# Kernel optimization log

Hardware: AMD Instinct MI355X
Metric: run time of the kernel (lower is better)

The kernel has to match this reference:

```python
import jax, jax.numpy as jnp
import numpy as np

B, L, NV = 16, 512, 321
D, PL, ST = 128, 16, 8
P = (L - PL) // ST + 2  # 64 patches (replication pad of `stride` on the right)
E, K, H = 8, 2, 512     # experts, top-n gates, expert hidden (4*d_model)
PRED = 96
BAL_COEF, Z_COEF = 0.01, 0.001


def sinusoidal_pe(n, d):
    pos = np.arange(n)[:, None].astype(np.float32)
    div = np.exp(np.arange(0, d, 2).astype(np.float32) * -(np.log(10000.0) / d))
    pe = np.zeros((n, d), dtype=np.float32)
    pe[:, 0::2] = np.sin(pos * div)
    pe[:, 1::2] = np.cos(pos * div)
    return jnp.asarray(pe)


def setup_inputs() -> dict:
    key = jax.random.key(0)
    ks = jax.random.split(key, 12)
    s = lambda i, shape, sc: jax.random.normal(ks[i], shape, jnp.float32) * sc
    return {
        "x_enc": jax.random.normal(ks[0], (B, L, NV), jnp.float32),
        "x_mark_enc": jax.random.normal(ks[1], (B, L, 4), jnp.float32),
        "x_dec": jax.random.normal(ks[2], (B, PRED, NV), jnp.float32),
        "x_mark_dec": jax.random.normal(ks[3], (B, PRED, 4), jnp.float32),
        "W_val": s(4, (PL, D), PL ** -0.5),
        "W_g": s(5, (D, E), D ** -0.5),
        "W1": s(6, (E, D, H), D ** -0.5),
        "b1": jnp.zeros((E, H), jnp.float32),
        "W2": s(7, (E, H, D), H ** -0.5),
        "b2": jnp.zeros((E, D), jnp.float32),
        "W_head": s(8, (D * P, PRED), (D * P) ** -0.5),
        "b_head": jnp.zeros((PRED,), jnp.float32),
    }


def _forward(x_enc, W_val, W_g, W1, b1, W2, b2, W_head, b_head):
    # RevIN-style instance norm (means detached as in torch .detach())
    means = jax.lax.stop_gradient(jnp.mean(x_enc, axis=1, keepdims=True))
    xc = x_enc - means
    stdev = jnp.sqrt(jnp.var(xc, axis=1, keepdims=True) + 1e-5)
    xn = xc / stdev

    # Patch embedding: [B, NV, L] -> replicate-pad -> unfold -> linear + sinusoidal PE
    x = jnp.transpose(xn, (0, 2, 1))                        # [B, NV, L]
    x = jnp.pad(x, ((0, 0), (0, 0), (0, ST)), mode="edge")  # ReplicationPad1d((0, stride))
    idx = np.arange(P)[:, None] * ST + np.arange(PL)        # [P, PL]
    patches = x[:, :, idx]                                  # [B, NV, P, PL]
    tok = patches.reshape(B * NV, P, PL)
    emb = tok @ W_val + sinusoidal_pe(P, D)[None]           # [N, P, D]

    # MoE: top-n softmax gating (gates not renormalized), balance + router-z aux losses
    t = emb.reshape(-1, D)                                  # [T, D], T = B*NV*P
    logits = t @ W_g                                        # [T, E]
    probs = jax.nn.softmax(logits, axis=-1)
    topv, topi = jax.lax.top_k(probs, K)                    # [T, K]

    out = jnp.zeros_like(t)
    for e in range(E):  # fixed small expert count; each expert is a GELU MLP
        h = jax.nn.gelu(t @ W1[e] + b1[e], approximate=False) @ W2[e] + b2[e]
        g = jnp.sum(jnp.where(topi == e, topv, 0.0), axis=-1)  # gate for expert e (0 if unrouted)
        out = out + g[:, None] * h

    me = jnp.mean(probs, axis=0)                                            # mean router prob per expert
    ce = jnp.mean(jax.nn.one_hot(topi, E, dtype=probs.dtype).sum(1), 0) / K  # dispatch fraction per expert
    balance_loss = E * jnp.sum(me * ce)
    z_loss = jnp.mean(jax.nn.logsumexp(logits, axis=-1) ** 2)
    aux = BAL_COEF * balance_loss + Z_COEF * z_loss

    # FlattenHead: [B, NV, P, D] -> [B, NV, D, P] -> flatten(-2) -> Linear(nf, pred_len)
    enc = out.reshape(B, NV, P, D).transpose(0, 1, 3, 2)    # [B, NV, D, P]
    dec = enc.reshape(B, NV, D * P) @ W_head + b_head        # [B, NV, PRED]
    dec = jnp.transpose(dec, (0, 2, 1))                      # [B, PRED, NV]

    # de-normalize
    dec = dec * stdev[:, 0][:, None, :] + means[:, 0][:, None, :]
    return dec, aux


def reference(x_enc, x_mark_enc, x_dec, x_mark_dec, W_val, W_g, W1, b1, W2, b2, W_head, b_head):
    return _forward(x_enc, W_val, W_g, W1, b1, W2, b2, W_head, b_head)
```

## Files before the change

kernel.cpp:

```cpp
#include <hip/hip_runtime.h>
#include <hip/hip_bf16.h>

typedef unsigned short u16;
typedef unsigned int   u32;
typedef unsigned long long u64;
typedef __attribute__((ext_vector_type(8))) short bf16x8;
typedef __attribute__((ext_vector_type(4))) float f32x4;
typedef __attribute__((ext_vector_type(16))) float f32x16;
typedef __attribute__((ext_vector_type(2))) unsigned int u32x2;

#define MFMA16(a,b,c) __builtin_amdgcn_mfma_f32_16x16x32_bf16(a,b,c,0,0,0)
#define MFMA32(a,b,c) __builtin_amdgcn_mfma_f32_32x32x16_bf16(a,b,c,0,0,0)

#define NV_   321
#define B_    16
#define L_    512
#define D_    128
#define P_    64
#define E_    8
#define H_    512
#define NRW   5136
#define NTOK  328704
#define DP_   8192
#define NBUCK 329728

static __device__ __forceinline__ u16 f2bf(float f){
  __hip_bfloat16 h = __float2bfloat16(f);
  return *reinterpret_cast<u16*>(&h);
}

static __device__ __forceinline__ float gelu_f(float x){
  float x2 = x*x;
  float p  = __builtin_fmaf(-0.1029433f, x2, -2.3022083f);
  float a  = x*p;
  float en = exp2f(a);
  float r  = __builtin_amdgcn_rcpf(1.0f + en);
  return x*r;
}

static constexpr size_t alup(size_t x){ return (x + 255) & ~(size_t)255; }
static constexpr size_t OFF_MEAN = 0;
static constexpr size_t OFF_RSTD = OFF_MEAN + alup((size_t)NRW*4);
static constexpr size_t OFF_STD  = OFF_RSTD + alup((size_t)NRW*4);
static constexpr size_t OFF_XT   = OFF_STD  + alup((size_t)NRW*4);
static constexpr size_t OFF_PE   = OFF_XT   + alup((size_t)NRW*L_*4);
static constexpr size_t OFF_W1T  = OFF_PE   + alup((size_t)P_*D_*4);
static constexpr size_t OFF_W2T  = OFF_W1T  + alup((size_t)E_*H_*D_*2);
static constexpr size_t OFF_WHT  = OFF_W2T  + alup((size_t)E_*D_*H_*2);
static constexpr size_t OFF_T    = OFF_WHT  + alup((size_t)96*DP_*2);
static constexpr size_t OFF_TOPI = OFF_T    + alup((size_t)NTOK*D_*2);
static constexpr size_t OFF_GATE = OFF_TOPI + alup((size_t)NTOK*4);
static constexpr size_t OFF_CNTR = OFF_GATE + alup((size_t)NTOK*8);
static constexpr size_t OFF_BTOK = OFF_CNTR + alup((size_t)1024);
static constexpr size_t OFF_BGT  = OFF_BTOK + alup((size_t)2*NBUCK*4);
static constexpr size_t OFF_OUT  = OFF_BGT  + alup((size_t)2*NBUCK*4);
static constexpr size_t OFF_MEAND= OFF_OUT  + alup((size_t)NTOK*D_*2);
static constexpr size_t OFF_RSTDD= OFF_MEAND+ alup((size_t)NRW*8);
static constexpr size_t OFF_WVG  = OFF_RSTDD+ alup((size_t)NRW*8);
static constexpr size_t OFF_PEG  = OFF_WVG  + alup((size_t)16*8*8);
static constexpr size_t OFF_PG   = OFF_PEG  + alup((size_t)P_*E_*8);
static constexpr size_t OFF_PI   = OFF_PG   + alup((size_t)NRW*12*4);



__global__ void k_xt(const float* __restrict__ x, float* __restrict__ xT){
  __shared__ float tile[32][33];
  int b = blockIdx.z;
  int v0 = blockIdx.x*32, l0 = blockIdx.y*32;
  int tx = threadIdx.x, ty = threadIdx.y;
  for(int i=ty;i<32;i+=8){
    int l = l0+i, v = v0+tx;
    tile[i][tx] = (v<NV_) ? x[((size_t)b*L_ + l)*NV_ + v] : 0.f;
  }
  __syncthreads();
  for(int i=ty;i<32;i+=8){
    int v = v0+i, l = l0+tx;
    if(v<NV_) xT[((size_t)(b*NV_+v))*L_ + l] = tile[tx][i];
  }
}

__global__ void k_stats(const float* __restrict__ xT, float* meanp, float* rstdp, float* stdp,
                        double* meand, double* rstdd){
  __shared__ double s1[256], s2[256];
  int r = blockIdx.x, t = threadIdx.x;
  double a = (double)xT[(size_t)r*L_ + t], b = (double)xT[(size_t)r*L_ + 256 + t];
  s1[t]=a+b; s2[t]=a*a+b*b;
  __syncthreads();
  for(int o=128;o>0;o>>=1){ if(t<o){ s1[t]+=s1[t+o]; s2[t]+=s2[t+o]; } __syncthreads(); }
  if(t==0){
    double m = s1[0]*(1.0/512.0);
    double var = s2[0]*(1.0/512.0) - m*m;
    double sd = sqrt(var + 1e-5);
    meanp[r]=(float)m; stdp[r]=(float)sd; rstdp[r]=(float)(1.0/sd);
    meand[r]=m; rstdd[r]=1.0/sd;
  }
}

__global__ void k_wprep(const float* __restrict__ Wval, const float* __restrict__ Wg,
                        const float* __restrict__ W1, const float* __restrict__ W2,
                        const float* __restrict__ Wh,
                        float* __restrict__ pef, double* __restrict__ Wvg,
                        double* __restrict__ peg,
                        u16* __restrict__ W1T, u16* __restrict__ W2T,
                        u16* __restrict__ WhT2){
  __shared__ float tile[32][33];
  int b = blockIdx.x;
  int tx = threadIdx.x, ty = threadIdx.y;
  int t = ty*32 + tx;
  if(b == 0){
    for(int i=t;i<8192;i+=256){
      int p = i>>7, d = i&127, k = d>>1;
      double div = exp(-(double)(2*k) * (9.210340371976184 /128.0));
      double ang = (double)p * div;
      double v = (d&1) ? cos(ang) : sin(ang);
      pef[i] = (float)v;
    }
    __syncthreads();
    if(t<128){
      int j = t>>3, e = t&7;
      double acc = 0.0;
      for(int d=0;d<128;d++) acc += (double)Wval[j*128+d] * (double)Wg[d*8+e];
      Wvg[t] = acc;
    }
    for(int q=t;q<512;q+=256){
      int p = q>>3, e = q&7;
      double acc = 0.0;
      for(int d=0;d<128;d++) acc += (double)pef[p*128+d] * (double)Wg[d*8+e];
      peg[q] = acc;
    }
    return;
  }
  if(b < 1025){
    bool isW1 = (b < 513);
    int rem = isW1 ? (b-1) : (b-513);
    int e = rem >> 6, r6 = rem & 63;
    int R = isW1 ? 128 : 512, C = isW1 ? 512 : 128;
    int c0 = (isW1 ? (r6 & 15) : (r6 & 3))*32;
    int r0 = (isW1 ? (r6 >> 4) : (r6 >> 2))*32;
    const float* src = (isW1 ? W1 : W2) + (size_t)e*R*C;
    u16* dst = (isW1 ? W1T : W2T) + (size_t)e*R*C;
    for(int i=ty;i<32;i+=8){
      int r=r0+i, c=c0+tx;
      tile[i][tx] = (r<R && c<C) ? src[(size_t)r*C+c] : 0.f;
    }
    __syncthreads();
    for(int i=ty;i<32;i+=8){
      int c=c0+i, r=r0+tx;
      if(c<C && r<R) dst[(size_t)c*R + r] = f2bf(tile[tx][i]);
    }
    return;
  }
  {
    int rem = b - 1025;
    int p = rem / 12, rr = rem - p*12;
    int d0 = (rr & 3)*32, o0 = (rr >> 2)*32;
    for(int i=ty;i<32;i+=8){
      int r = (d0+i)*64 + p;
      tile[i][tx] = Wh[(size_t)r*96 + o0 + tx];
    }
    __syncthreads();
    for(int i=ty;i<32;i+=8){
      int o = o0+i;
      WhT2[(size_t)o*DP_ + p*128 + d0 + tx] = f2bf(tile[tx][i]);
    }
  }
}

__global__ __launch_bounds__(256) void k_embed(
    const float* __restrict__ xT, const float* __restrict__ meanp, const float* __restrict__ rstdp,
    const float* __restrict__ Wval, const float* __restrict__ pe,
    u16* __restrict__ tglob)
{
  __shared__ __align__(16) float xn[520];
  int r = blockIdx.x, t = threadIdx.x;
  float mean = meanp[r], rstd = rstdp[r];
  float v0 = (xT[(size_t)r*L_ + t]       - mean)*rstd;
  float v1 = (xT[(size_t)r*L_ + 256 + t] - mean)*rstd;
  xn[t] = v0; xn[t+256] = v1;
  if(t==255){
    #pragma unroll
    for(int i=512;i<520;i++) xn[i]=v1;
  }
  int d0 = (t & 63)*2;
  int p0 = t >> 6;
  float2 w[16];
  #pragma unroll
  for(int j=0;j<16;j++) w[j] = *(const float2*)(Wval + j*128 + d0);
  __syncthreads();

  for(int p=p0;p<64;p+=4){
    const float4* xp = (const float4*)(xn + p*8);
    float4 x0=xp[0], x1=xp[1], x2=xp[2], x3=xp[3];
    float xv[16];
    *(float4*)(xv+0)=x0; *(float4*)(xv+4)=x1; *(float4*)(xv+8)=x2; *(float4*)(xv+12)=x3;
    float2 pw = *(const float2*)(pe + p*128 + d0);
    float a0 = pw.x, a1 = pw.y;
    #pragma unroll
    for(int j=0;j<16;j++){ a0 += xv[j]*w[j].x; a1 += xv[j]*w[j].y; }
    u32 packed = (u32)f2bf(a0) | ((u32)f2bf(a1)<<16);
    *(u32*)(tglob + ((size_t)(r*64+p)*128 + d0)) = packed;
  }
}

__global__ __launch_bounds__(256) void k_gate(
    const float* __restrict__ xT, const double* __restrict__ meand, const double* __restrict__ rstdd,
    const double* __restrict__ Wvg, const double* __restrict__ peg,
    int* __restrict__ topip, float2* __restrict__ gatep,
    float* __restrict__ pg, int* __restrict__ pib)
{
  __shared__ double xn[520];
  __shared__ double lgt[64][9];
  int r = blockIdx.x, t = threadIdx.x;
  double m = meand[r], rs = rstdd[r];
  double v0 = ((double)xT[(size_t)r*L_ + t]       - m)*rs;
  double v1 = ((double)xT[(size_t)r*L_ + 256 + t] - m)*rs;
  xn[t]=v0; xn[t+256]=v1;
  if(t==255){
    #pragma unroll
    for(int i=512;i<520;i++) xn[i]=v1;
  }
  __syncthreads();
  for(int q=t;q<512;q+=256){
    int p = q>>3, e = q&7;
    double acc = peg[q];
    #pragma unroll
    for(int j=0;j<16;j++) acc += xn[p*8+j]*Wvg[j*8+e];
    lgt[p][e] = acc;
  }
  __syncthreads();
  if(t<64){
    int token = r*64 + t;
    double l0[8];
    #pragma unroll
    for(int e=0;e<8;e++) l0[e]=lgt[t][e];
    double mx=l0[0];
    #pragma unroll
    for(int e=1;e<8;e++) mx = fmax(mx,l0[e]);
    int i1=0; double b1v=l0[0];
    #pragma unroll
    for(int e=1;e<8;e++) if(l0[e]>b1v){b1v=l0[e]; i1=e;}
    int i2=-1; double b2v=-1e300;
    #pragma unroll
    for(int e=0;e<8;e++) if(e!=i1 && l0[e]>b2v){b2v=l0[e]; i2=e;}
    float pr[8]; float sum=0.f;
    #pragma unroll
    for(int e=0;e<8;e++){ pr[e]=__expf((float)(l0[e]-mx)); sum+=pr[e]; }
    float inv = 1.f/sum;
    #pragma unroll
    for(int e=0;e<8;e++) pr[e]*=inv;
    topip[token] = i1 | (i2<<8);
    gatep[token] = make_float2(pr[i1], pr[i2]);
    float lse = (float)mx + __logf(sum);
    #pragma unroll
    for(int e=0;e<8;e++){
      float v = pr[e];
      for(int o=32;o>0;o>>=1) v += __shfl_down(v,o);
      if(t==0) pg[r*12+e] = v;
    }
    {
      float z = lse*lse;
      for(int o=32;o>0;o>>=1) z += __shfl_down(z,o);
      if(t==0) pg[r*12+8] = z;
    }
    #pragma unroll
    for(int e=0;e<8;e++){
      u64 m1 = __ballot(i1==e);
      u64 m2 = __ballot(i2==e);
      if(t==0){
        pib[r*16+e]   = (int)__popcll(m1);
        pib[r*16+8+e] = (int)__popcll(m2);
      }
    }
  }
}

__global__ __launch_bounds__(256) void k_aux(const float* __restrict__ pg, const int* __restrict__ pib,
                                             int* __restrict__ ci, float* __restrict__ dout){
  __shared__ double sd[256];
  __shared__ int si[256];
  __shared__ double totd[9];
  __shared__ int toti[16];
  int t = threadIdx.x;
  double accd[9]; int acci[16];
  #pragma unroll
  for(int c=0;c<9;c++) accd[c]=0.0;
  #pragma unroll
  for(int c=0;c<16;c++) acci[c]=0;
  for(int r=t;r<NRW;r+=256){
    #pragma unroll
    for(int c=0;c<9;c++) accd[c] += (double)pg[r*12+c];
    #pragma unroll
    for(int c=0;c<16;c++) acci[c] += pib[r*16+c];
  }
  for(int c=0;c<9;c++){
    sd[t]=accd[c]; __syncthreads();
    for(int o=128;o>0;o>>=1){ if(t<o) sd[t]+=sd[t+o]; __syncthreads(); }
    if(t==0) totd[c]=sd[0];
    __syncthreads();
  }
  for(int c=0;c<16;c++){
    si[t]=acci[c]; __syncthreads();
    for(int o=128;o>0;o>>=1){ if(t<o) si[t]+=si[t+o]; __syncthreads(); }
    if(t==0) toti[c]=si[0];
    __syncthreads();
  }
  if(t==0){
    const double invN = 1.0/(double)NTOK;
    double bal = 0.0;
    int es1=0, bs1=0, es2=0, bs2=0;
    for(int e=0;e<8;e++){
      int c1 = toti[e], c2 = toti[8+e];
      bal += (totd[e]*invN) * ((double)(c1+c2) * invN * 0.5);
      ci[32+e]=es1; ci[16+e]=es1; ci[50+e]=bs1;
      ci[41+e]=es2; ci[24+e]=es2; ci[59+e]=bs2;
      es1 += c1; bs1 += (c1+127)>>7;
      es2 += c2; bs2 += (c2+127)>>7;
    }
    ci[40]=es1; ci[58]=bs1;
    ci[49]=es2; ci[67]=bs2;
    dout[493056] = (float)(0.01*8.0*bal + 0.001*(totd[8]*invN));
  }
}

__global__ __launch_bounds__(256) void k_scatter(const int* __restrict__ topip,
    const float2* __restrict__ gatep, int* __restrict__ ci,
    int* __restrict__ btok, float* __restrict__ bgt){
  __shared__ int lc[16]; __shared__ int lb[16];
  int t = threadIdx.x;
  int token = blockIdx.x*256 + t;
  if(t<16) lc[t]=0;
  __syncthreads();
  int ti = topip[token];
  float2 g = gatep[token];
  int e1 = ti & 255, e2 = (ti>>8)&255;
  int r1 = atomicAdd(&lc[e1],1);
  int r2 = atomicAdd(&lc[8+e2],1);
  __syncthreads();
  if(t<8)            lb[t] = atomicAdd(&ci[16+t],   lc[t]);
  else if(t<16)      lb[t] = atomicAdd(&ci[24+t-8], lc[t]);
  __syncthreads();
  int p1 = lb[e1]+r1, p2 = lb[8+e2]+r2;
  btok[p1] = token;         bgt[p1] = g.x;
  btok[NBUCK+p2] = token;   bgt[NBUCK+p2] = g.y;
}

static __device__ __forceinline__ f32x16 acc1_init(const float* b1l, int hc, int hi){
  f32x16 a;
  const float* bp = b1l + hc*32 + 4*hi;
  #pragma unroll
  for(int qq=0;qq<4;qq++){
    f32x4 b4 = *(const f32x4*)(bp + 8*qq);
    a[4*qq+0]=b4.x; a[4*qq+1]=b4.y; a[4*qq+2]=b4.z; a[4*qq+3]=b4.w;
  }
  return a;
}

static __device__ __forceinline__ void gelu_pack(const f32x16& acc1, bf16x8& fA, bf16x8& fB){
  u32 pk[8];
  #pragma unroll
  for(int i=0;i<8;i++){
    float g0 = gelu_f(acc1[2*i]);
    float g1 = gelu_f(acc1[2*i+1]);
    asm("v_cvt_pk_bf16_f32 %0, %1, %2" : "=v"(pk[i]) : "v"(g0), "v"(g1));
  }
  union { bf16x8 v; u32 w[4]; } uA, uB;
  u32x2 s02 = __builtin_amdgcn_permlane32_swap(pk[0], pk[2], false, false);
  u32x2 s13 = __builtin_amdgcn_permlane32_swap(pk[1], pk[3], false, false);
  u32x2 s46 = __builtin_amdgcn_permlane32_swap(pk[4], pk[6], false, false);
  u32x2 s57 = __builtin_amdgcn_permlane32_swap(pk[5], pk[7], false, false);
  uA.w[0]=s02.x; uA.w[1]=s13.x; uA.w[2]=s02.y; uA.w[3]=s13.y;
  uB.w[0]=s46.x; uB.w[1]=s57.x; uB.w[2]=s46.y; uB.w[3]=s57.y;
  fA = uA.v; fB = uB.v;
}

__global__ __launch_bounds__(256,3) void k_expert(
    const u16* __restrict__ tglob,
    const u16* __restrict__ W1T, const u16* __restrict__ W2T,
    const float* __restrict__ b1g, const float* __restrict__ b2g,
    const int* __restrict__ ci,
    const int* __restrict__ btok, const float* __restrict__ bgt,
    u16* __restrict__ outg, int slot)
{
  __shared__ __align__(16) u16 W1b[2][4352];
  __shared__ __align__(16) u16 W2b[2][5120];
  __shared__ __align__(16) float b1l[512];

  int bid = blockIdx.x, t = threadIdx.x;
  int stB = 32 + slot*9, bsB = 50 + slot*9;
  int boff = slot*NBUCK;
  if(bid >= ci[bsB+8]) return;
  int e = 0;
  #pragma unroll
  for(int k2=1;k2<8;k2++) if(bid >= ci[bsB+k2]) e = k2;
  int row0 = ci[stB+e] + (bid - ci[bsB+e])*128;
  int rend = ci[stB+e+1];

  int wid = t>>6, lane = t&63;
  int m = lane&31, hi = lane>>5;
  int rb = wid*32;

  int hr = t>>3, q = t&7;
  int dr = t>>1, q2 = t&1;

  {
    const u16* s1 = W1T + ((size_t)e*H_ + hr)*128 + q*16;
    uint4 p0 = *(const uint4*)(s1);
    uint4 p1 = *(const uint4*)(s1+8);
    u16* d1 = &W1b[0][hr*136 + q*16];
    *(uint4*)(d1)   = p0;
    *(uint4*)(d1+8) = p1;
    if(t<128){
      float4 bv = *(const float4*)(b1g + e*H_ + t*4);
      *(float4*)(b1l + t*4) = bv;
    }
  }

  int posA = row0 + rb + m;
  bool valA = posA < rend;
  int tokA  = valA ? btok[boff+posA] : 0;
  float gt  = valA ? bgt[boff+posA]  : 0.f;
  const u16* arow = tglob + (size_t)tokA*128 + hi*8;
  bf16x8 areg[8];
  #pragma unroll
  for(int ks=0;ks<8;ks++) areg[ks] = *(const bf16x8*)(arow + ks*16);

  f32x16 accO[4];
  #pragma unroll
  for(int nt=0;nt<4;nt++){
    const float* bp2 = b2g + e*D_ + nt*32 + 4*hi;
    #pragma unroll
    for(int qq=0;qq<4;qq++){
      float4 b4 = *(const float4*)(bp2 + 8*qq);
      accO[nt][4*qq+0]=b4.x; accO[nt][4*qq+1]=b4.y;
      accO[nt][4*qq+2]=b4.z; accO[nt][4*qq+3]=b4.w;
    }
  }
  __syncthreads();

  bf16x8 fA, fB;
  {
    const u16* s1 = W1T + ((size_t)e*H_ + 32 + hr)*128 + q*16;
    uint4 l0 = *(const uint4*)(s1), l1 = *(const uint4*)(s1+8);
    const u16* s2 = W2T + ((size_t)e*D_ + dr)*H_ + q2*16;
    uint4 l2 = *(const uint4*)(s2), l3 = *(const uint4*)(s2+8);
    f32x16 acc1 = acc1_init(b1l, 0, hi);
    __builtin_amdgcn_s_setprio(1);
    #pragma unroll
    for(int ks=0;ks<8;ks++){
      bf16x8 wa = *(const bf16x8*)(&W1b[0][0] + m*136 + ks*16 + hi*8);
      acc1 = MFMA32(wa, areg[ks], acc1);
    }
    __builtin_amdgcn_s_setprio(0);
    u16* d1 = &W1b[1][hr*136 + q*16];
    *(uint4*)(d1)   = l0; *(uint4*)(d1+8) = l1;
    u16* d2 = &W2b[0][dr*40 + q2*16];
    *(uint4*)(d2)   = l2; *(uint4*)(d2+8) = l3;
    gelu_pack(acc1, fA, fB);
    __syncthreads();
  }
  for(int hc=1; hc<16; hc++){
    uint4 l0, l1;
    if(hc<15){
      const u16* s1 = W1T + ((size_t)e*H_ + (hc+1)*32 + hr)*128 + q*16;
      l0 = *(const uint4*)(s1); l1 = *(const uint4*)(s1+8);
    }
    const u16* s2 = W2T + ((size_t)e*D_ + dr)*H_ + hc*32 + q2*16;
    uint4 l2 = *(const uint4*)(s2), l3 = *(const uint4*)(s2+8);
    f32x16 acc1 = acc1_init(b1l, hc, hi);
    const u16* W1c = &W1b[hc&1][0];
    const u16* W2p = &W2b[(hc-1)&1][0];
    __builtin_amdgcn_s_setprio(1);
    #pragma unroll
    for(int ks=0;ks<8;ks++){
      bf16x8 wa = *(const bf16x8*)(W1c + m*136 + ks*16 + hi*8);
      acc1 = MFMA32(wa, areg[ks], acc1);
      bf16x8 a2 = *(const bf16x8*)(W2p + ((ks&3)*32+m)*40 + (ks>>2)*16 + hi*8);
      accO[ks&3] = MFMA32(a2, (ks>>2)?fB:fA, accO[ks&3]);
    }
    __builtin_amdgcn_s_setprio(0);
    if(hc<15){
      u16* d1 = &W1b[(hc+1)&1][hr*136 + q*16];
      *(uint4*)(d1)   = l0; *(uint4*)(d1+8) = l1;
    }
    u16* d2 = &W2b[hc&1][dr*40 + q2*16];
    *(uint4*)(d2)   = l2; *(uint4*)(d2+8) = l3;
    gelu_pack(acc1, fA, fB);
    __syncthreads();
  }
  {
    const u16* W2p = &W2b[1][0];
    __builtin_amdgcn_s_setprio(1);
    #pragma unroll
    for(int ks=0;ks<8;ks++){
      bf16x8 a2 = *(const bf16x8*)(W2p + ((ks&3)*32+m)*40 + (ks>>2)*16 + hi*8);
      accO[ks&3] = MFMA32(a2, (ks>>2)?fB:fA, accO[ks&3]);
    }
    __builtin_amdgcn_s_setprio(0);
  }

  if(valA){
    u16* obase = outg + (size_t)tokA*128 + 4*hi;
    #pragma unroll
    for(int nt=0;nt<4;nt++){
      #pragma unroll
      for(int qq=0;qq<4;qq++){
        float v0 = accO[nt][4*qq+0]*gt;
        float v1 = accO[nt][4*qq+1]*gt;
        float v2 = accO[nt][4*qq+2]*gt;
        float v3 = accO[nt][4*qq+3]*gt;
        u32* dp = (u32*)(obase + nt*32 + 8*qq);
        if(slot==1){
          u32x2 old = *(const u32x2*)dp;
          v0 += __uint_as_float(old.x<<16);
          v1 += __uint_as_float(old.x & 0xffff0000u);
          v2 += __uint_as_float(old.y<<16);
          v3 += __uint_as_float(old.y & 0xffff0000u);
        }
        u32 w0, w1;
        asm("v_cvt_pk_bf16_f32 %0, %1, %2" : "=v"(w0) : "v"(v0), "v"(v1));
        asm("v_cvt_pk_bf16_f32 %0, %1, %2" : "=v"(w1) : "v"(v2), "v"(v3));
        u32x2 nv; nv.x = w0; nv.y = w1;
        *(u32x2*)dp = nv;
      }
    }
  }
}

__global__ __launch_bounds__(256) void k_head(const u16* __restrict__ Aout,
    const u16* __restrict__ WhT2, float* __restrict__ dec8){
  int bid = blockIdx.x;
  int mb = bid>>3, kseg = bid&7;
  int t = threadIdx.x, wid = t>>6, lane = t&63;
  int quad = lane>>4, li = lane&15;
  int r0 = mb*64 + wid*16;
  int rowA = r0 + li; if(rowA >= NRW) rowA = NRW-1;
  const u16* aptr = Aout + (size_t)rowA*DP_ + kseg*1024 + quad*8;
  const u16* bptr = WhT2 + (size_t)li*DP_  + kseg*1024 + quad*8;
  f32x4 acc[6];
  #pragma unroll
  for(int j=0;j<6;j++) acc[j]=(f32x4){0,0,0,0};
  #pragma unroll 4
  for(int ks=0;ks<32;ks++){
    bf16x8 af = *(const bf16x8*)(aptr + ks*32);
    #pragma unroll
    for(int nt=0;nt<6;nt++){
      bf16x8 bw = *(const bf16x8*)(bptr + (size_t)nt*16*DP_ + ks*32);
      acc[nt] = MFMA16(af, bw, acc[nt]);
    }
  }
  float* dst = dec8 + (size_t)kseg*NRW*96;
  #pragma unroll
  for(int nt=0;nt<6;nt++)
    #pragma unroll
    for(int rg=0;rg<4;rg++){
      int mm = r0 + quad*4 + rg;
      if(mm < NRW) dst[(size_t)mm*96 + nt*16 + li] = acc[nt][rg];
    }
}

__global__ void k_final(const float* __restrict__ dec8, const float* __restrict__ bhead,
    const float* __restrict__ stdp, const float* __restrict__ meanp, float* __restrict__ outp){
  __shared__ float s[64*97];
  int b = blockIdx.y, v0 = blockIdx.x*64;
  int t = threadIdx.x;
  for(int i=t;i<6144;i+=256){
    int vi = i/96, o = i - vi*96;
    int v = v0+vi;
    float acc = 0.f;
    if(v<NV_){
      size_t base = (size_t)(b*NV_+v)*96 + o;
      #pragma unroll
      for(int ks=0;ks<8;ks++) acc += dec8[(size_t)ks*NRW*96 + base];
    }
    s[vi*97+o] = acc;
  }
  __syncthreads();
  for(int i=t;i<6144;i+=256){
    int o = i>>6, vi = i&63;
    int v = v0+vi;
    if(v<NV_){
      int r = b*NV_+v;
      outp[((size_t)b*96 + o)*NV_ + v] = (s[vi*97+o] + bhead[o])*stdp[r] + meanp[r];
    }
  }
}

extern "C" void kernel_launch(void* const* d_in, const int* in_sizes, int n_in,
                              void* d_out, int out_size, void* d_ws, size_t ws_size,
                              hipStream_t stream){
  const float* x_enc = (const float*)d_in[0];
  const float* W_val = (const float*)d_in[4];
  const float* W_g   = (const float*)d_in[5];
  const float* W1    = (const float*)d_in[6];
  const float* b1    = (const float*)d_in[7];
  const float* W2    = (const float*)d_in[8];
  const float* b2    = (const float*)d_in[9];
  const float* W_head= (const float*)d_in[10];
  const float* b_head= (const float*)d_in[11];
  float* outp = (float*)d_out;
  char* ws = (char*)d_ws;

  float* meanp = (float*)(ws+OFF_MEAN);
  float* rstdp = (float*)(ws+OFF_RSTD);
  float* stdp  = (float*)(ws+OFF_STD);
  float* xT    = (float*)(ws+OFF_XT);
  float* pe    = (float*)(ws+OFF_PE);
  u16*   W1T   = (u16*)(ws+OFF_W1T);
  u16*   W2T   = (u16*)(ws+OFF_W2T);
  u16*   WhT2  = (u16*)(ws+OFF_WHT);
  u16*   tglob = (u16*)(ws+OFF_T);
  float* dec8  = (float*)(ws+OFF_T);
  int*   topip = (int*)(ws+OFF_TOPI);
  float2* gatep= (float2*)(ws+OFF_GATE);
  int*   ci    = (int*)(ws+OFF_CNTR+128);
  int*   btok  = (int*)(ws+OFF_BTOK);
  float* bgt   = (float*)(ws+OFF_BGT);
  u16*   outg  = (u16*)(ws+OFF_OUT);
  double* meand= (double*)(ws+OFF_MEAND);
  double* rstdd= (double*)(ws+OFF_RSTDD);
  double* Wvg  = (double*)(ws+OFF_WVG);
  double* peg  = (double*)(ws+OFF_PEG);
  float* pg    = (float*)(ws+OFF_PG);
  int*   pib   = (int*)(ws+OFF_PI);

  hipMemsetAsync(ws+OFF_CNTR, 0, 1024, stream);

  k_xt<<<dim3(11,16,B_), dim3(32,8), 0, stream>>>(x_enc, xT);
  k_stats<<<NRW, 256, 0, stream>>>(xT, meanp, rstdp, stdp, meand, rstdd);
  k_wprep<<<1793, dim3(32,8), 0, stream>>>(W_val, W_g, W1, W2, W_head,
                                           pe, Wvg, peg, W1T, W2T, WhT2);
  k_embed<<<NRW, 256, 0, stream>>>(xT, meanp, rstdp, W_val, pe, tglob);
  k_gate<<<NRW, 256, 0, stream>>>(xT, meand, rstdd, Wvg, peg, topip, gatep, pg, pib);
  k_aux<<<1, 256, 0, stream>>>(pg, pib, ci, outp);
  k_scatter<<<NTOK/256, 256, 0, stream>>>(topip, gatep, ci, btok, bgt);
  k_expert<<<2576, 256, 0, stream>>>(tglob, W1T, W2T, b1, b2, ci, btok, bgt, outg, 0);
  k_expert<<<2576, 256, 0, stream>>>(tglob, W1T, W2T, b1, b2, ci, btok, bgt, outg, 1);
  k_head<<<648, 256, 0, stream>>>(outg, WhT2, dec8);
  k_final<<<dim3(6,B_), 256, 0, stream>>>(dec8, b_head, stdp, meanp, outp);
}
```

Before: 622.2 us.

## Merge both expert-slot launches into one, writing separate buffers summed in head

The two k_expert launches for top-1 and top-2 slots become one grid of twice the size, with each block deriving its slot from blockIdx. Slot-1 no longer does a read-modify-write on the shared output. Each slot writes its own bf16 buffer, and k_head loads both and adds them before the MFMA. This removes a kernel boundary and the dependent read from the expert epilogue, so the two slots can overlap and tail idle time shrinks. The cost is doubled A-operand traffic in k_head, plus an extra workspace buffer that aliases the transient xT/topi/gate regions. It also adds double bf16 rounding where there used to be one.

```diff
diff --git a/kernel.cpp b/kernel.cpp
--- a/kernel.cpp
+++ b/kernel.cpp
@@ -23,10 +23,17 @@
 #define NTOK  328704
 #define DP_   8192
 #define NBUCK 329728
+#define NBLK_SLOT 2576
 
 static __device__ __forceinline__ u16 f2bf(float f){
   __hip_bfloat16 h = __float2bfloat16(f);
   return *reinterpret_cast<u16*>(&h);
+}
+
+static __device__ __forceinline__ u32 bfadd2(u32 a, u32 b){
+  float lo = __uint_as_float(a<<16)           + __uint_as_float(b<<16);
+  float hi = __uint_as_float(a&0xffff0000u)   + __uint_as_float(b&0xffff0000u);
+  return (u32)f2bf(lo) | ((u32)f2bf(hi)<<16);
 }
 
 static __device__ __forceinline__ float gelu_f(float x){
@@ -42,24 +49,27 @@
 static constexpr size_t OFF_MEAN = 0;
 static constexpr size_t OFF_RSTD = OFF_MEAN + alup((size_t)NRW*4);
 static constexpr size_t OFF_STD  = OFF_RSTD + alup((size_t)NRW*4);
-static constexpr size_t OFF_XT   = OFF_STD  + alup((size_t)NRW*4);
-static constexpr size_t OFF_PE   = OFF_XT   + alup((size_t)NRW*L_*4);
-static constexpr size_t OFF_W1T  = OFF_PE   + alup((size_t)P_*D_*4);
+static constexpr size_t OFF_MEAND= OFF_STD  + alup((size_t)NRW*4);
+static constexpr size_t OFF_RSTDD= OFF_MEAND+ alup((size_t)NRW*8);
+static constexpr size_t OFF_WVG  = OFF_RSTDD+ alup((size_t)NRW*8);
+static constexpr size_t OFF_PEG  = OFF_WVG  + alup((size_t)16*8*8);
+static constexpr size_t OFF_W1T  = OFF_PEG  + alup((size_t)P_*E_*8);
 static constexpr size_t OFF_W2T  = OFF_W1T  + alup((size_t)E_*H_*D_*2);
 static constexpr size_t OFF_WHT  = OFF_W2T  + alup((size_t)E_*D_*H_*2);
 static constexpr size_t OFF_T    = OFF_WHT  + alup((size_t)96*DP_*2);
-static constexpr size_t OFF_TOPI = OFF_T    + alup((size_t)NTOK*D_*2);
-static constexpr size_t OFF_GATE = OFF_TOPI + alup((size_t)NTOK*4);
-static constexpr size_t OFF_CNTR = OFF_GATE + alup((size_t)NTOK*8);
+static constexpr size_t OFF_CNTR = OFF_T    + alup((size_t)NTOK*D_*2);
 static constexpr size_t OFF_BTOK = OFF_CNTR + alup((size_t)1024);
 static constexpr size_t OFF_BGT  = OFF_BTOK + alup((size_t)2*NBUCK*4);
 static constexpr size_t OFF_OUT  = OFF_BGT  + alup((size_t)2*NBUCK*4);
-static constexpr size_t OFF_MEAND= OFF_OUT  + alup((size_t)NTOK*D_*2);
-static constexpr size_t OFF_RSTDD= OFF_MEAND+ alup((size_t)NRW*8);
-static constexpr size_t OFF_WVG  = OFF_RSTDD+ alup((size_t)NRW*8);
-static constexpr size_t OFF_PEG  = OFF_WVG  + alup((size_t)16*8*8);
-static constexpr size_t OFF_PG   = OFF_PEG  + alup((size_t)P_*E_*8);
+static constexpr size_t OFF_OUT2 = OFF_OUT  + alup((size_t)NTOK*D_*2);
+static constexpr size_t OFF_XT   = OFF_OUT2;
+static constexpr size_t OFF_PE   = OFF_XT   + alup((size_t)NRW*L_*4);
+static constexpr size_t OFF_TOPI = OFF_PE   + alup((size_t)P_*D_*4);
+static constexpr size_t OFF_GATE = OFF_TOPI + alup((size_t)NTOK*4);
+static constexpr size_t OFF_PG   = OFF_GATE + alup((size_t)NTOK*8);
 static constexpr size_t OFF_PI   = OFF_PG   + alup((size_t)NRW*12*4);
+static_assert(OFF_PI + (size_t)NRW*16*4 <= OFF_OUT2 + (size_t)NTOK*D_*2,
+              "transients must fit inside outg2 alias region");
 
 
 
@@ -379,13 +389,15 @@
     const float* __restrict__ b1g, const float* __restrict__ b2g,
     const int* __restrict__ ci,
     const int* __restrict__ btok, const float* __restrict__ bgt,
-    u16* __restrict__ outg, int slot)
+    u16* __restrict__ outg, u16* __restrict__ outg2)
 {
   __shared__ __align__(16) u16 W1b[2][4352];
   __shared__ __align__(16) u16 W2b[2][5120];
   __shared__ __align__(16) float b1l[512];
 
-  int bid = blockIdx.x, t = threadIdx.x;
+  int bid0 = blockIdx.x, t = threadIdx.x;
+  int slot = (bid0 >= NBLK_SLOT) ? 1 : 0;
+  int bid  = bid0 - slot*NBLK_SLOT;
   int stB = 32 + slot*9, bsB = 50 + slot*9;
   int boff = slot*NBUCK;
   if(bid >= ci[bsB+8]) return;
@@ -499,7 +511,7 @@
   }
 
   if(valA){
-    u16* obase = outg + (size_t)tokA*128 + 4*hi;
+    u16* obase = (slot ? outg2 : outg) + (size_t)tokA*128 + 4*hi;
     #pragma unroll
     for(int nt=0;nt<4;nt++){
       #pragma unroll
@@ -508,25 +520,18 @@
         float v1 = accO[nt][4*qq+1]*gt;
         float v2 = accO[nt][4*qq+2]*gt;
         float v3 = accO[nt][4*qq+3]*gt;
-        u32* dp = (u32*)(obase + nt*32 + 8*qq);
-        if(slot==1){
-          u32x2 old = *(const u32x2*)dp;
-          v0 += __uint_as_float(old.x<<16);
-          v1 += __uint_as_float(old.x & 0xffff0000u);
-          v2 += __uint_as_float(old.y<<16);
-          v3 += __uint_as_float(old.y & 0xffff0000u);
-        }
         u32 w0, w1;
         asm("v_cvt_pk_bf16_f32 %0, %1, %2" : "=v"(w0) : "v"(v0), "v"(v1));
         asm("v_cvt_pk_bf16_f32 %0, %1, %2" : "=v"(w1) : "v"(v2), "v"(v3));
         u32x2 nv; nv.x = w0; nv.y = w1;
-        *(u32x2*)dp = nv;
+        *(u32x2*)(obase + nt*32 + 8*qq) = nv;
       }
     }
   }
 }
 
 __global__ __launch_bounds__(256) void k_head(const u16* __restrict__ Aout,
+    const u16* __restrict__ Aout2,
     const u16* __restrict__ WhT2, float* __restrict__ dec8){
   int bid = blockIdx.x;
   int mb = bid>>3, kseg = bid&7;
@@ -534,14 +539,23 @@
   int quad = lane>>4, li = lane&15;
   int r0 = mb*64 + wid*16;
   int rowA = r0 + li; if(rowA >= NRW) rowA = NRW-1;
-  const u16* aptr = Aout + (size_t)rowA*DP_ + kseg*1024 + quad*8;
+  size_t abase = (size_t)rowA*DP_ + kseg*1024 + quad*8;
+  const u16* aptr  = Aout  + abase;
+  const u16* aptr2 = Aout2 + abase;
   const u16* bptr = WhT2 + (size_t)li*DP_  + kseg*1024 + quad*8;
   f32x4 acc[6];
   #pragma unroll
   for(int j=0;j<6;j++) acc[j]=(f32x4){0,0,0,0};
   #pragma unroll 4
   for(int ks=0;ks<32;ks++){
-    bf16x8 af = *(const bf16x8*)(aptr + ks*32);
+    uint4 va = *(const uint4*)(aptr  + ks*32);
+    uint4 vb = *(const uint4*)(aptr2 + ks*32);
+    union { uint4 u; bf16x8 v; } vs;
+    vs.u.x = bfadd2(va.x, vb.x);
+    vs.u.y = bfadd2(va.y, vb.y);
+    vs.u.z = bfadd2(va.z, vb.z);
+    vs.u.w = bfadd2(va.w, vb.w);
+    bf16x8 af = vs.v;
     #pragma unroll
     for(int nt=0;nt<6;nt++){
       bf16x8 bw = *(const bf16x8*)(bptr + (size_t)nt*16*DP_ + ks*32);
@@ -616,6 +630,7 @@
   int*   btok  = (int*)(ws+OFF_BTOK);
   float* bgt   = (float*)(ws+OFF_BGT);
   u16*   outg  = (u16*)(ws+OFF_OUT);
+  u16*   outg2 = (u16*)(ws+OFF_OUT2);
   double* meand= (double*)(ws+OFF_MEAND);
   double* rstdd= (double*)(ws+OFF_RSTDD);
   double* Wvg  = (double*)(ws+OFF_WVG);
@@ -633,8 +648,8 @@
   k_gate<<<NRW, 256, 0, stream>>>(xT, meand, rstdd, Wvg, peg, topip, gatep, pg, pib);
   k_aux<<<1, 256, 0, stream>>>(pg, pib, ci, outp);
   k_scatter<<<NTOK/256, 256, 0, stream>>>(topip, gatep, ci, btok, bgt);
-  k_expert<<<2576, 256, 0, stream>>>(tglob, W1T, W2T, b1, b2, ci, btok, bgt, outg, 0);
-  k_expert<<<2576, 256, 0, stream>>>(tglob, W1T, W2T, b1, b2, ci, btok, bgt, outg, 1);
-  k_head<<<648, 256, 0, stream>>>(outg, WhT2, dec8);
+  k_expert<<<2*NBLK_SLOT, 256, 0, stream>>>(tglob, W1T, W2T, b1, b2, ci, btok, bgt,
+                                            outg, outg2);
+  k_head<<<648, 256, 0, stream>>>(outg, outg2, WhT2, dec8);
   k_final<<<dim3(6,B_), 256, 0, stream>>>(dec8, b_head, stdp, meanp, outp);
 }
```

After: 605.0 us. -2.8%, faster.
